# Performance work log

Hardware: AMD Instinct MI355X
Metric: run time of the kernel (lower is better)

Reference implementation:

```python
import jax, jax.numpy as jnp
import numpy as np

NEG_INF = -1e30  # large negative in place of -inf for masked scores (fp32-safe)


def setup_inputs() -> dict:
    key = jax.random.key(0)
    kq, kk, kv, km = jax.random.split(key, 4)
    B, H, S, D = 2, 16, 2048, 64
    query = jax.random.normal(kq, (B, H, S, D), dtype=jnp.float32)
    k = jax.random.normal(kk, (B, H, S, D), dtype=jnp.float32)
    v = jax.random.normal(kv, (B, H, S, D), dtype=jnp.float32)
    mask = jax.random.randint(km, (B, H, S, S), 0, 2, dtype=jnp.int32)
    return {"query": query, "key": k, "value": v, "mask": mask}


def reference(query, key, value, mask):
    # Online-softmax chunked attention is mathematically exact softmax attention;
    # we compute the equivalent masked softmax attention in one fused expression.
    d_k = query.shape[-1]
    scale = 1.0 / np.sqrt(d_k).astype(np.float32)
    # scores: [B, H, Sq, Sk]
    scores = jnp.einsum('bhqd,bhkd->bhqk', query, key) * scale
    scores = jnp.where(mask == 0, NEG_INF, scores)
    attn = jax.nn.softmax(scores, axis=-1)
    out = jnp.einsum('bhqk,bhkd->bhqd', attn, value)
    return out
```

## Files before the change

### kernel.cpp

```cpp
#include <hip/hip_runtime.h>


typedef __attribute__((ext_vector_type(8))) short bf16x8;
typedef __attribute__((ext_vector_type(4))) short s16x4;
typedef __attribute__((ext_vector_type(4))) float f32x4;

#define S_LEN 2048
#define NT 32
#define PP 72
#define QSCALE 0.1803368801f

__device__ __forceinline__ short f2bf(float f) {
    union { float f; unsigned u; } v; v.f = f;
    unsigned r = v.u + 0x7fffu + ((v.u >> 16) & 1u);
    return (short)(r >> 16);
}

__device__ __forceinline__ float fexp2(float x) {
#if __has_builtin(__builtin_amdgcn_exp2f)
    return __builtin_amdgcn_exp2f(x);
#else
    return exp2f(x);
#endif
}

#if __has_builtin(__builtin_amdgcn_cvt_pk_bf16_f32)
typedef __attribute__((ext_vector_type(2))) __bf16 bf16x2_t;
__device__ __forceinline__ unsigned pk2(float a, float b) {
    bf16x2_t v = __builtin_amdgcn_cvt_pk_bf16_f32(a, b);
    union { bf16x2_t v; unsigned u; } u; u.v = v; return u.u;
}
#else
__device__ __forceinline__ unsigned pk2(float a, float b) {
    return (unsigned)(unsigned short)f2bf(a) | ((unsigned)(unsigned short)f2bf(b) << 16);
}
#endif

__device__ __forceinline__ bf16x8 cvt8(float4 a, float4 b, float s) {
    bf16x8 f;
    f[0]=f2bf(a.x*s); f[1]=f2bf(a.y*s); f[2]=f2bf(a.z*s); f[3]=f2bf(a.w*s);
    f[4]=f2bf(b.x*s); f[5]=f2bf(b.y*s); f[6]=f2bf(b.z*s); f[7]=f2bf(b.w*s);
    return f;
}

__global__ __launch_bounds__(256)
void pack_all(const float* __restrict__ Q, const float* __restrict__ K,
              const float* __restrict__ V, short* __restrict__ Qw,
              short* __restrict__ Kw, short* __restrict__ Vw) {
    __shared__ float vt[64][65];
    const int bh = blockIdx.x, t = blockIdx.y, which = blockIdx.z;
    if (which == 0) {
        for (int ci = threadIdx.x; ci < 512; ci += 256) {
            int ww = ci >> 7, ks = (ci >> 6) & 1, lane = ci & 63;
            int quad = lane >> 4, c = lane & 15;
            int row = t * 64 + ww * 16 + c;
            int d0 = ks * 32 + quad * 8;
            const float* src = Q + ((size_t)(bh * S_LEN + row)) * 64 + d0;
            float4 a = *(const float4*)src;
            float4 b = *(const float4*)(src + 4);
            *(bf16x8*)(Qw + ((size_t)(bh * 32 + t) * 512 + ci) * 8) = cvt8(a, b, QSCALE);
        }
    } else if (which == 1) {
        for (int ci = threadIdx.x; ci < 512; ci += 256) {
            int fb = ci >> 6, lane = ci & 63;
            int nb = fb >> 1, ks = fb & 1;
            int quad = lane >> 4, c = lane & 15;
            int key = t * 64 + c * 4 + nb;
            int d0 = ks * 32 + quad * 8;
            const float* src = K + ((size_t)(bh * S_LEN + key)) * 64 + d0;
            float4 a = *(const float4*)src;
            float4 b = *(const float4*)(src + 4);
            *(bf16x8*)(Kw + ((size_t)(bh * 32 + t) * 512 + ci) * 8) = cvt8(a, b, 1.0f);
        }
    } else {
        {
            int key = threadIdx.x >> 2, d0 = (threadIdx.x & 3) * 16;
            const float* src = V + ((size_t)(bh * S_LEN + t * 64 + key)) * 64 + d0;
            float4 a = *(const float4*)src;
            float4 b = *(const float4*)(src + 4);
            float4 cc = *(const float4*)(src + 8);
            float4 d = *(const float4*)(src + 12);
            float* dst = &vt[key][d0];
            dst[0]=a.x; dst[1]=a.y; dst[2]=a.z; dst[3]=a.w;
            dst[4]=b.x; dst[5]=b.y; dst[6]=b.z; dst[7]=b.w;
            dst[8]=cc.x; dst[9]=cc.y; dst[10]=cc.z; dst[11]=cc.w;
            dst[12]=d.x; dst[13]=d.y; dst[14]=d.z; dst[15]=d.w;
        }
        __syncthreads();
        for (int ci = threadIdx.x; ci < 512; ci += 256) {
            int fb = ci >> 6, lane = ci & 63;
            int db = fb >> 1, ks = fb & 1;
            int quad = lane >> 4, c = lane & 15;
            bf16x8 f;
#pragma unroll
            for (int j = 0; j < 8; ++j) {
                int pos = ks * 32 + quad * 8 + j;
                f[j] = f2bf(vt[pos][db * 16 + c]);
            }
            *(bf16x8*)(Vw + ((size_t)(bh * 32 + t) * 512 + ci) * 8) = f;
        }
    }
}

typedef __attribute__((address_space(3))) unsigned lds_u32;
typedef const __attribute__((address_space(1))) unsigned glob_u32;

#define MFMA(a, b, acc) __builtin_amdgcn_mfma_f32_16x16x32_bf16(a, b, acc, 0, 0, 0)

__global__ __launch_bounds__(256, 2)
void fa_main(const short* __restrict__ Qw, const short* __restrict__ Kw,
             const short* __restrict__ Vw, const int* __restrict__ M,
             float* __restrict__ O) {
    __shared__ __align__(16) short Kb[2 * 8 * 512];
    __shared__ __align__(16) short Vb[2 * 8 * 512];
    __shared__ __align__(16) short Pwv[8 * 16 * PP];

    const int tid  = threadIdx.x;
    const int lane = tid & 63;
    const int w    = tid >> 6;
    const int quad = lane >> 4;
    const int c    = lane & 15;

    const int bid = blockIdx.x;
    const int x = bid & 7, y = bid >> 3;
    const int bh = x * 4 + (y >> 4);
    const int p  = y & 15;

    bf16x8 qf[2][2];
#pragma unroll
    for (int s = 0; s < 2; ++s) {
        const short* qb = Qw + ((size_t)(bh * 32 + 2 * p + s) * 512 + w * 128 + lane) * 8;
        qf[s][0] = *(const bf16x8*)qb;
        qf[s][1] = *(const bf16x8*)(qb + 512);
    }

    const bool isK = (w < 2);
    const short* gsrc = (isK ? Kw : Vw) + (size_t)bh * 32 * 4096 + (w & 1) * 2048 + (size_t)lane * 8;
    short* ldst0 = (isK ? Kb : Vb) + (w & 1) * 2048;

    const int* mrow[2];
    mrow[0] = M + ((size_t)(bh * S_LEN + p * 128 + w * 16 + quad * 4)) * S_LEN + 4 * c;
    mrow[1] = mrow[0] + (size_t)64 * S_LEN;

    f32x4 acco[2][4];
    float lacc[2][4];
#pragma unroll
    for (int s = 0; s < 2; ++s)
#pragma unroll
        for (int r = 0; r < 4; ++r) {
            lacc[s][r] = 0.f;
            acco[s][r][0]=0.f; acco[s][r][1]=0.f; acco[s][r][2]=0.f; acco[s][r][3]=0.f;
        }

    if (isK) {
#pragma unroll
        for (int i = 0; i < 4; ++i)
            __builtin_amdgcn_global_load_lds((glob_u32*)(gsrc + i * 512),
                                             (lds_u32*)(ldst0 + i * 512), 16, 0, 0);
    }
    int4 mcur[2][4];
#pragma unroll
    for (int s = 0; s < 2; ++s)
#pragma unroll
        for (int r = 0; r < 4; ++r)
            mcur[s][r] = *(const int4*)(mrow[s] + (size_t)r * S_LEN);
    __syncthreads();

    short* pw[2];
    pw[0] = &Pwv[(0 + w) * 16 * PP];
    pw[1] = &Pwv[(4 + w) * 16 * PP];
    const short* pr0 = pw[0] + c * PP;
    const short* pr1 = pw[1] + c * PP;

    for (int t = 0; t < NT; ++t) {
        const int tn = (t + 1) & (NT - 1);
        const int dtile = isK ? tn : t;
        const int dbuf = (dtile & 1) * 4096;
#pragma unroll
        for (int i = 0; i < 4; ++i)
            __builtin_amdgcn_global_load_lds((glob_u32*)(gsrc + (size_t)dtile * 4096 + i * 512),
                                             (lds_u32*)(ldst0 + dbuf + i * 512), 16, 0, 0);
        int4 mnxt[2][4];
#pragma unroll
        for (int s = 0; s < 2; ++s)
#pragma unroll
            for (int r = 0; r < 4; ++r)
                mnxt[s][r] = *(const int4*)(mrow[s] + (size_t)r * S_LEN + tn * 64);

        const int kc = (t & 1) * 4096;
        f32x4 accs[2][4];
#pragma unroll
        for (int s = 0; s < 2; ++s)
#pragma unroll
            for (int nb = 0; nb < 4; ++nb) { accs[s][nb][0]=0.f; accs[s][nb][1]=0.f; accs[s][nb][2]=0.f; accs[s][nb][3]=0.f; }
#pragma unroll
        for (int nb = 0; nb < 4; ++nb) {
            bf16x8 b0 = *(const bf16x8*)&Kb[kc + (nb * 2 + 0) * 512 + lane * 8];
            bf16x8 b1 = *(const bf16x8*)&Kb[kc + (nb * 2 + 1) * 512 + lane * 8];
            accs[0][nb] = MFMA(qf[0][0], b0, accs[0][nb]);
            accs[0][nb] = MFMA(qf[0][1], b1, accs[0][nb]);
            accs[1][nb] = MFMA(qf[1][0], b0, accs[1][nb]);
            accs[1][nb] = MFMA(qf[1][1], b1, accs[1][nb]);
        }

        if (t > 0) {
            const int vc = ((t - 1) & 1) * 4096;
            bf16x8 pf00 = *(const bf16x8*)(pr0 + quad * 8);
            bf16x8 pf01 = *(const bf16x8*)(pr0 + 32 + quad * 8);
            bf16x8 pf10 = *(const bf16x8*)(pr1 + quad * 8);
            bf16x8 pf11 = *(const bf16x8*)(pr1 + 32 + quad * 8);
#pragma unroll
            for (int db = 0; db < 4; ++db) {
                bf16x8 v0 = *(const bf16x8*)&Vb[vc + (db * 2 + 0) * 512 + lane * 8];
                bf16x8 v1 = *(const bf16x8*)&Vb[vc + (db * 2 + 1) * 512 + lane * 8];
                acco[0][db] = MFMA(pf00, v0, acco[0][db]);
                acco[0][db] = MFMA(pf01, v1, acco[0][db]);
                acco[1][db] = MFMA(pf10, v0, acco[1][db]);
                acco[1][db] = MFMA(pf11, v1, acco[1][db]);
            }
        }

#pragma unroll
        for (int s = 0; s < 2; ++s) {
            short* pws = pw[s];
#pragma unroll
            for (int r = 0; r < 4; ++r) {
                const int4 mm = mcur[s][r];
                float e0 = fexp2(accs[s][0][r]); e0 = (mm.x != 0) ? e0 : 0.f;
                float e1 = fexp2(accs[s][1][r]); e1 = (mm.y != 0) ? e1 : 0.f;
                float e2 = fexp2(accs[s][2][r]); e2 = (mm.z != 0) ? e2 : 0.f;
                float e3 = fexp2(accs[s][3][r]); e3 = (mm.w != 0) ? e3 : 0.f;
                lacc[s][r] += (e0 + e1) + (e2 + e3);
                union { unsigned u[2]; s16x4 v; } pk;
                pk.u[0] = pk2(e0, e1);
                pk.u[1] = pk2(e2, e3);
                *(s16x4*)&pws[(quad * 4 + r) * PP + 4 * c] = pk.v;
            }
        }
#pragma unroll
        for (int s = 0; s < 2; ++s)
#pragma unroll
            for (int r = 0; r < 4; ++r) mcur[s][r] = mnxt[s][r];
        __syncthreads();
    }

    {
        const int vc = ((NT - 1) & 1) * 4096;
        bf16x8 pf00 = *(const bf16x8*)(pr0 + quad * 8);
        bf16x8 pf01 = *(const bf16x8*)(pr0 + 32 + quad * 8);
        bf16x8 pf10 = *(const bf16x8*)(pr1 + quad * 8);
        bf16x8 pf11 = *(const bf16x8*)(pr1 + 32 + quad * 8);
#pragma unroll
        for (int db = 0; db < 4; ++db) {
            bf16x8 v0 = *(const bf16x8*)&Vb[vc + (db * 2 + 0) * 512 + lane * 8];
            bf16x8 v1 = *(const bf16x8*)&Vb[vc + (db * 2 + 1) * 512 + lane * 8];
            acco[0][db] = MFMA(pf00, v0, acco[0][db]);
            acco[0][db] = MFMA(pf01, v1, acco[0][db]);
            acco[1][db] = MFMA(pf10, v0, acco[1][db]);
            acco[1][db] = MFMA(pf11, v1, acco[1][db]);
        }
    }

#pragma unroll
    for (int s = 0; s < 2; ++s) {
        float* orow = O + ((size_t)(bh * S_LEN + p * 128 + s * 64 + w * 16 + quad * 4)) * 64 + c;
#pragma unroll
        for (int r = 0; r < 4; ++r) {
            float l = lacc[s][r];
            l += __shfl_xor(l, 1);
            l += __shfl_xor(l, 2);
            l += __shfl_xor(l, 4);
            l += __shfl_xor(l, 8);
            float inv = 1.0f / l;
#pragma unroll
            for (int db = 0; db < 4; ++db)
                orow[(size_t)r * 64 + db * 16] = acco[s][db][r] * inv;
        }
    }
}

extern "C" void kernel_launch(void* const* d_in, const int* in_sizes, int n_in,
                              void* d_out, int out_size, void* d_ws, size_t ws_size,
                              hipStream_t stream) {
    const float* Q = (const float*)d_in[0];
    const float* K = (const float*)d_in[1];
    const float* V = (const float*)d_in[2];
    const int*   M = (const int*)d_in[3];
    float* O = (float*)d_out;

    short* Qw = (short*)d_ws;
    short* Kw = Qw + (size_t)32 * 32 * 4096;
    short* Vw = Kw + (size_t)32 * 32 * 4096;

    hipLaunchKernelGGL(pack_all, dim3(32, 32, 3), dim3(256), 0, stream, Q, K, V, Qw, Kw, Vw);
    hipLaunchKernelGGL(fa_main, dim3(512), dim3(256), 0, stream, Qw, Kw, Vw, M, O);
}
```

Baseline: 752.7 us.

## Fuse Q conversion into attention kernel, stage K via LDS, nontemporal mask loads

Removes the separate Q packing pass. The attention kernel now loads fp32 Q directly and converts it to bf16 fragments in registers, so the Qw workspace is no longer written and read back. K packing now goes through the LDS tile with coalesced row loads, the same way V already did. The int mask, the dominant memory stream, is read with nontemporal loads to reduce cache pollution. The first K prefetch is issued before the Q loads so the two overlap.

```diff
diff --git a/kernel.cpp b/kernel.cpp
--- a/kernel.cpp
+++ b/kernel.cpp
@@ -4,6 +4,7 @@
 typedef __attribute__((ext_vector_type(8))) short bf16x8;
 typedef __attribute__((ext_vector_type(4))) short s16x4;
 typedef __attribute__((ext_vector_type(4))) float f32x4;
+typedef __attribute__((ext_vector_type(4))) int   i32x4;
 
 #define S_LEN 2048
 #define NT 32
@@ -36,6 +37,14 @@
 }
 #endif
 
+__device__ __forceinline__ i32x4 ntload4(const int* p) {
+#if __has_builtin(__builtin_nontemporal_load)
+    return __builtin_nontemporal_load((const i32x4*)p);
+#else
+    return *(const i32x4*)p;
+#endif
+}
+
 __device__ __forceinline__ bf16x8 cvt8(float4 a, float4 b, float s) {
     bf16x8 f;
     f[0]=f2bf(a.x*s); f[1]=f2bf(a.y*s); f[2]=f2bf(a.z*s); f[3]=f2bf(a.w*s);
@@ -44,59 +53,45 @@
 }
 
 __global__ __launch_bounds__(256)
-void pack_all(const float* __restrict__ Q, const float* __restrict__ K,
-              const float* __restrict__ V, short* __restrict__ Qw,
-              short* __restrict__ Kw, short* __restrict__ Vw) {
+void pack_kv(const float* __restrict__ K, const float* __restrict__ V,
+             short* __restrict__ Kw, short* __restrict__ Vw) {
     __shared__ float vt[64][65];
     const int bh = blockIdx.x, t = blockIdx.y, which = blockIdx.z;
+    const float* src_mat = (which == 0) ? K : V;
+    {
+        int row = threadIdx.x >> 2, d0 = (threadIdx.x & 3) * 16;
+        const float* src = src_mat + ((size_t)(bh * S_LEN + t * 64 + row)) * 64 + d0;
+        float4 a = *(const float4*)src;
+        float4 b = *(const float4*)(src + 4);
+        float4 cc = *(const float4*)(src + 8);
+        float4 d = *(const float4*)(src + 12);
+        float* dst = &vt[row][d0];
+        dst[0]=a.x; dst[1]=a.y; dst[2]=a.z; dst[3]=a.w;
+        dst[4]=b.x; dst[5]=b.y; dst[6]=b.z; dst[7]=b.w;
+        dst[8]=cc.x; dst[9]=cc.y; dst[10]=cc.z; dst[11]=cc.w;
+        dst[12]=d.x; dst[13]=d.y; dst[14]=d.z; dst[15]=d.w;
+    }
+    __syncthreads();
     if (which == 0) {
-        for (int ci = threadIdx.x; ci < 512; ci += 256) {
-            int ww = ci >> 7, ks = (ci >> 6) & 1, lane = ci & 63;
-            int quad = lane >> 4, c = lane & 15;
-            int row = t * 64 + ww * 16 + c;
-            int d0 = ks * 32 + quad * 8;
-            const float* src = Q + ((size_t)(bh * S_LEN + row)) * 64 + d0;
-            float4 a = *(const float4*)src;
-            float4 b = *(const float4*)(src + 4);
-            *(bf16x8*)(Qw + ((size_t)(bh * 32 + t) * 512 + ci) * 8) = cvt8(a, b, QSCALE);
-        }
-    } else if (which == 1) {
         for (int ci = threadIdx.x; ci < 512; ci += 256) {
             int fb = ci >> 6, lane = ci & 63;
             int nb = fb >> 1, ks = fb & 1;
             int quad = lane >> 4, c = lane & 15;
-            int key = t * 64 + c * 4 + nb;
-            int d0 = ks * 32 + quad * 8;
-            const float* src = K + ((size_t)(bh * S_LEN + key)) * 64 + d0;
-            float4 a = *(const float4*)src;
-            float4 b = *(const float4*)(src + 4);
-            *(bf16x8*)(Kw + ((size_t)(bh * 32 + t) * 512 + ci) * 8) = cvt8(a, b, 1.0f);
+            bf16x8 f;
+#pragma unroll
+            for (int j = 0; j < 8; ++j)
+                f[j] = f2bf(vt[c * 4 + nb][ks * 32 + quad * 8 + j]);
+            *(bf16x8*)(Kw + ((size_t)(bh * 32 + t) * 512 + ci) * 8) = f;
         }
     } else {
-        {
-            int key = threadIdx.x >> 2, d0 = (threadIdx.x & 3) * 16;
-            const float* src = V + ((size_t)(bh * S_LEN + t * 64 + key)) * 64 + d0;
-            float4 a = *(const float4*)src;
-            float4 b = *(const float4*)(src + 4);
-            float4 cc = *(const float4*)(src + 8);
-            float4 d = *(const float4*)(src + 12);
-            float* dst = &vt[key][d0];
-            dst[0]=a.x; dst[1]=a.y; dst[2]=a.z; dst[3]=a.w;
-            dst[4]=b.x; dst[5]=b.y; dst[6]=b.z; dst[7]=b.w;
-            dst[8]=cc.x; dst[9]=cc.y; dst[10]=cc.z; dst[11]=cc.w;
-            dst[12]=d.x; dst[13]=d.y; dst[14]=d.z; dst[15]=d.w;
-        }
-        __syncthreads();
         for (int ci = threadIdx.x; ci < 512; ci += 256) {
             int fb = ci >> 6, lane = ci & 63;
             int db = fb >> 1, ks = fb & 1;
             int quad = lane >> 4, c = lane & 15;
             bf16x8 f;
 #pragma unroll
-            for (int j = 0; j < 8; ++j) {
-                int pos = ks * 32 + quad * 8 + j;
-                f[j] = f2bf(vt[pos][db * 16 + c]);
-            }
+            for (int j = 0; j < 8; ++j)
+                f[j] = f2bf(vt[ks * 32 + quad * 8 + j][db * 16 + c]);
             *(bf16x8*)(Vw + ((size_t)(bh * 32 + t) * 512 + ci) * 8) = f;
         }
     }
@@ -108,7 +103,7 @@
 #define MFMA(a, b, acc) __builtin_amdgcn_mfma_f32_16x16x32_bf16(a, b, acc, 0, 0, 0)
 
 __global__ __launch_bounds__(256, 2)
-void fa_main(const short* __restrict__ Qw, const short* __restrict__ Kw,
+void fa_main(const float* __restrict__ Q, const short* __restrict__ Kw,
              const short* __restrict__ Vw, const int* __restrict__ M,
              float* __restrict__ O) {
     __shared__ __align__(16) short Kb[2 * 8 * 512];
@@ -126,18 +121,29 @@
     const int bh = x * 4 + (y >> 4);
     const int p  = y & 15;
 
-    bf16x8 qf[2][2];
-#pragma unroll
-    for (int s = 0; s < 2; ++s) {
-        const short* qb = Qw + ((size_t)(bh * 32 + 2 * p + s) * 512 + w * 128 + lane) * 8;
-        qf[s][0] = *(const bf16x8*)qb;
-        qf[s][1] = *(const bf16x8*)(qb + 512);
-    }
-
     const bool isK = (w < 2);
     const short* gsrc = (isK ? Kw : Vw) + (size_t)bh * 32 * 4096 + (w & 1) * 2048 + (size_t)lane * 8;
     short* ldst0 = (isK ? Kb : Vb) + (w & 1) * 2048;
 
+    if (isK) {
+#pragma unroll
+        for (int i = 0; i < 4; ++i)
+            __builtin_amdgcn_global_load_lds((glob_u32*)(gsrc + i * 512),
+                                             (lds_u32*)(ldst0 + i * 512), 16, 0, 0);
+    }
+
+    bf16x8 qf[2][2];
+#pragma unroll
+    for (int s = 0; s < 2; ++s) {
+        const float* qp = Q + ((size_t)(bh * S_LEN + p * 128 + s * 64 + w * 16 + c)) * 64 + quad * 8;
+#pragma unroll
+        for (int ks = 0; ks < 2; ++ks) {
+            float4 a = *(const float4*)(qp + ks * 32);
+            float4 b = *(const float4*)(qp + ks * 32 + 4);
+            qf[s][ks] = cvt8(a, b, QSCALE);
+        }
+    }
+
     const int* mrow[2];
     mrow[0] = M + ((size_t)(bh * S_LEN + p * 128 + w * 16 + quad * 4)) * S_LEN + 4 * c;
     mrow[1] = mrow[0] + (size_t)64 * S_LEN;
@@ -152,18 +158,12 @@
             acco[s][r][0]=0.f; acco[s][r][1]=0.f; acco[s][r][2]=0.f; acco[s][r][3]=0.f;
         }
 
-    if (isK) {
-#pragma unroll
-        for (int i = 0; i < 4; ++i)
-            __builtin_amdgcn_global_load_lds((glob_u32*)(gsrc + i * 512),
-                                             (lds_u32*)(ldst0 + i * 512), 16, 0, 0);
-    }
-    int4 mcur[2][4];
+    i32x4 mcur[2][4];
 #pragma unroll
     for (int s = 0; s < 2; ++s)
 #pragma unroll
         for (int r = 0; r < 4; ++r)
-            mcur[s][r] = *(const int4*)(mrow[s] + (size_t)r * S_LEN);
+            mcur[s][r] = ntload4(mrow[s] + (size_t)r * S_LEN);
     __syncthreads();
 
     short* pw[2];
@@ -180,12 +180,12 @@
         for (int i = 0; i < 4; ++i)
             __builtin_amdgcn_global_load_lds((glob_u32*)(gsrc + (size_t)dtile * 4096 + i * 512),
                                              (lds_u32*)(ldst0 + dbuf + i * 512), 16, 0, 0);
-        int4 mnxt[2][4];
+        i32x4 mnxt[2][4];
 #pragma unroll
         for (int s = 0; s < 2; ++s)
 #pragma unroll
             for (int r = 0; r < 4; ++r)
-                mnxt[s][r] = *(const int4*)(mrow[s] + (size_t)r * S_LEN + tn * 64);
+                mnxt[s][r] = ntload4(mrow[s] + (size_t)r * S_LEN + tn * 64);
 
         const int kc = (t & 1) * 4096;
         f32x4 accs[2][4];
@@ -225,11 +225,11 @@
             short* pws = pw[s];
 #pragma unroll
             for (int r = 0; r < 4; ++r) {
-                const int4 mm = mcur[s][r];
-                float e0 = fexp2(accs[s][0][r]); e0 = (mm.x != 0) ? e0 : 0.f;
-                float e1 = fexp2(accs[s][1][r]); e1 = (mm.y != 0) ? e1 : 0.f;
-                float e2 = fexp2(accs[s][2][r]); e2 = (mm.z != 0) ? e2 : 0.f;
-                float e3 = fexp2(accs[s][3][r]); e3 = (mm.w != 0) ? e3 : 0.f;
+                const i32x4 mm = mcur[s][r];
+                float e0 = fexp2(accs[s][0][r]); e0 = (mm[0] != 0) ? e0 : 0.f;
+                float e1 = fexp2(accs[s][1][r]); e1 = (mm[1] != 0) ? e1 : 0.f;
+                float e2 = fexp2(accs[s][2][r]); e2 = (mm[2] != 0) ? e2 : 0.f;
+                float e3 = fexp2(accs[s][3][r]); e3 = (mm[3] != 0) ? e3 : 0.f;
                 lacc[s][r] += (e0 + e1) + (e2 + e3);
                 union { unsigned u[2]; s16x4 v; } pk;
                 pk.u[0] = pk2(e0, e1);
@@ -288,10 +288,9 @@
     const int*   M = (const int*)d_in[3];
     float* O = (float*)d_out;
 
-    short* Qw = (short*)d_ws;
-    short* Kw = Qw + (size_t)32 * 32 * 4096;
+    short* Kw = (short*)d_ws;
     short* Vw = Kw + (size_t)32 * 32 * 4096;
 
-    hipLaunchKernelGGL(pack_all, dim3(32, 32, 3), dim3(256), 0, stream, Q, K, V, Qw, Kw, Vw);
-    hipLaunchKernelGGL(fa_main, dim3(512), dim3(256), 0, stream, Qw, Kw, Vw, M, O);
-}
+    hipLaunchKernelGGL(pack_kv, dim3(32, 32, 2), dim3(256), 0, stream, K, V, Kw, Vw);
+    hipLaunchKernelGGL(fa_main, dim3(512), dim3(256), 0, stream, Q, Kw, Vw, M, O);
+}
```

New measurement: 728.7 us. 1.03x faster.
